# Kernel optimization log

Measured on AMD Instinct MI355X. Metric: run time of the kernel, lower is better.

Reference implementation:

```python
import jax, jax.numpy as jnp
import numpy as np

B, N, C = 16, 65536, 21          # batch, anchors, classes (class 0 = background)
TH_CONF = 0.05                   # confidence threshold
TH_IOU = 0.5                     # NMS IoU threshold
TOP_K = 200                      # candidates kept per (batch, class) before NMS
V0, V1 = 0.1, 0.2                # SSD box-coder variances


def setup_inputs() -> dict:
    key = jax.random.key(0)
    k1, k2, k3, k4 = jax.random.split(key, 4)
    conf = jax.random.normal(k1, (B, N, C), dtype=jnp.float32)
    loc = jax.random.normal(k2, (B, N, 4), dtype=jnp.float32)
    # anchors in center form (cx, cy, w, h), normalized coords
    cxcy = jax.random.uniform(k3, (N, 2), dtype=jnp.float32)
    wh = 0.02 + 0.2 * jax.random.uniform(k4, (N, 2), dtype=jnp.float32)
    anchors = jnp.concatenate([cxcy, wh], axis=-1)
    return {"conf": conf, "loc": loc, "anchors": anchors}


def _decode(anchors, loc):
    # SSD decode: anchors [N,4] center form, loc [B,N,4] offsets -> [B,N,4] xyxy
    a_xy, a_wh = anchors[:, :2], anchors[:, 2:]
    xy = a_xy + loc[..., :2] * V0 * a_wh
    wh = a_wh * jnp.exp(loc[..., 2:] * V1)
    return jnp.concatenate([xy - 0.5 * wh, xy + 0.5 * wh], axis=-1)


def _iou(boxes):
    # boxes [K,4] xyxy -> pairwise IoU [K,K]
    area = jnp.maximum(boxes[:, 2] - boxes[:, 0], 0.0) * jnp.maximum(boxes[:, 3] - boxes[:, 1], 0.0)
    lt = jnp.maximum(boxes[:, None, :2], boxes[None, :, :2])
    rb = jnp.minimum(boxes[:, None, 2:], boxes[None, :, 2:])
    wh = jnp.maximum(rb - lt, 0.0)
    inter = wh[..., 0] * wh[..., 1]
    union = area[:, None] + area[None, :] - inter
    return inter / jnp.maximum(union, 1e-9)


def _nms_keep(iou, valid):
    # greedy NMS over score-sorted candidates; valid = (score >= TH_CONF)
    K = iou.shape[0]
    idx = jnp.arange(K)

    def body(keep, xs):
        row, v, i = xs
        suppressed = jnp.any((row > TH_IOU) & keep & (idx < i))
        k = v & (~suppressed)
        return keep.at[i].set(k), 0

    keep, _ = jax.lax.scan(body, jnp.zeros((K,), dtype=bool), (iou, valid, idx))
    return keep


def reference(conf, loc, anchors):
    score = jax.nn.softmax(conf, axis=2)            # [B,N,C]
    boxes = _decode(anchors, loc)                   # [B,N,4]
    # skip background class 0 (cls_base = 1 for softmax classifier)
    cls_scores = jnp.swapaxes(score[..., 1:], 1, 2)  # [B,C-1,N]
    top_s, top_i = jax.lax.top_k(cls_scores, TOP_K)  # [B,C-1,K], sorted desc
    top_boxes = jax.vmap(lambda bx, ix: bx[ix])(boxes, top_i)  # [B,C-1,K,4]
    valid = top_s >= TH_CONF
    keep = jax.vmap(jax.vmap(lambda b, v: _nms_keep(_iou(b), v)))(top_boxes, valid)  # [B,C-1,K]
    out_boxes = jnp.where(keep[..., None], top_boxes, 0.0)
    out_scores = jnp.where(keep, top_s, 0.0)
    return jnp.concatenate([out_boxes, out_scores[..., None]], axis=-1)  # [B,C-1,K,5]
```

## Files before the change

### kernel.cpp

```cpp
#include <hip/hip_runtime.h>
#include <stdint.h>

#define NB     16
#define NANCH  65536
#define NC     21
#define NCLS   20
#define NCOL   (NB * NCLS)
#define TOPK   200
#define NBINS  1024
#define CAP    256
#define CAPCOL 4096
#define CNTSTRIDE 16
#define NPAIRS 19900

constexpr float TH      = 0.05f;
constexpr float TPRE    = 0.15f;
constexpr float SCALE15 = (float)NBINS / 0.85f;
constexpr float SCALE05 = (float)NBINS / 0.95f;

__device__ __forceinline__ int bin15(float s) {
  int b = (int)((s - 0.15f) * SCALE15);
  return b < 0 ? 0 : (b > NBINS - 1 ? NBINS - 1 : b);
}
__device__ __forceinline__ int bin05(float s) {
  int b = (int)((s - 0.05f) * SCALE05);
  return b < 0 ? 0 : (b > NBINS - 1 ? NBINS - 1 : b);
}

__device__ __forceinline__ unsigned long long shflx64(unsigned long long v, int m) {
  unsigned int lo = (unsigned int)v, hi = (unsigned int)(v >> 32);
  lo = __shfl_xor(lo, m);
  hi = __shfl_xor(hi, m);
  return ((unsigned long long)hi << 32) | lo;
}
__device__ __forceinline__ unsigned long long shfl64(unsigned long long v, int src) {
  unsigned int lo = (unsigned int)v, hi = (unsigned int)(v >> 32);
  lo = (unsigned int)__shfl((int)lo, src);
  hi = (unsigned int)__shfl((int)hi, src);
  return ((unsigned long long)hi << 32) | lo;
}

__device__ __forceinline__ void softmax_tail(const float* x, float* e, float& S) {
  float m = x[0];
#pragma unroll
  for (int c = 1; c < NC; ++c) m = fmaxf(m, x[c]);
#pragma unroll
  for (int c = 0; c < NC; ++c) e[c] = expf(x[c] - m);
  float r0 = e[0] + e[8],  r1 = e[1] + e[9],  r2 = e[2] + e[10], r3 = e[3] + e[11];
  float r4 = e[4] + e[12], r5 = e[5] + e[13], r6 = e[6] + e[14], r7 = e[7] + e[15];
  S = ((r0 + r1) + (r2 + r3)) + ((r4 + r5) + (r6 + r7));
  S += e[16]; S += e[17]; S += e[18]; S += e[19]; S += e[20];
}

__global__ __launch_bounds__(256) void softmax_collect_kernel(
    const float* __restrict__ conf,
    unsigned int* __restrict__ cnt, unsigned long long* __restrict__ cand) {
  const int tid = threadIdx.x;
  __shared__ float ld[256 * NC];
  const float4* src = (const float4*)conf + (long long)blockIdx.x * 1344;
  float4* dst4 = (float4*)ld;
#pragma unroll
  for (int i = 0; i < 5; ++i) dst4[tid + i * 256] = src[tid + i * 256];
  if (tid < 64) dst4[tid + 1280] = src[tid + 1280];
  __syncthreads();

  const int a = blockIdx.x * 256 + tid;
  const int b = a >> 16;
  const int n = a & (NANCH - 1);
  float x[NC];
#pragma unroll
  for (int c = 0; c < NC; ++c) x[c] = ld[tid * NC + c];
  float e[NC], S;
  softmax_tail(x, e, S);
  const float t = TPRE * S;
  unsigned int takemask = 0;
#pragma unroll
  for (int c = 0; c < NCLS; ++c)
    if (e[c + 1] >= t) takemask |= (1u << c);

  __shared__ unsigned int wcnt[4][NCLS];
  __shared__ unsigned int wbase[4][NCLS];
  const int wave = tid >> 6, lane = tid & 63;
#pragma unroll
  for (int c = 0; c < NCLS; ++c) {
    unsigned long long m = __ballot((takemask >> c) & 1);
    if (lane == 0) wcnt[wave][c] = (unsigned int)__popcll(m);
  }
  __syncthreads();
  if (tid < NCLS) {
    const int c = tid;
    unsigned int t0 = wcnt[0][c], t1 = wcnt[1][c], t2 = wcnt[2][c], t3 = wcnt[3][c];
    unsigned int tot = t0 + t1 + t2 + t3;
    unsigned int base = tot ? atomicAdd(&cnt[(b * NCLS + c) * CNTSTRIDE], tot) : 0u;
    wbase[0][c] = base;
    wbase[1][c] = base + t0;
    wbase[2][c] = base + t0 + t1;
    wbase[3][c] = base + t0 + t1 + t2;
  }
  __syncthreads();
#pragma unroll
  for (int c = 0; c < NCLS; ++c) {
    bool take = (takemask >> c) & 1;
    unsigned long long m = __ballot(take);
    if (take) {
      float s = e[c + 1] / S;
      unsigned int off = wbase[wave][c] +
                         (unsigned int)__popcll(m & ((1ULL << lane) - 1));
      if (off < CAPCOL) {
        unsigned int key = __float_as_uint(s) | 0x80000000u;
        cand[(long long)(b * NCLS + c) * CAPCOL + off] =
            ((unsigned long long)(key ^ 0xFFFFFFFFu) << 32) |
            (unsigned long long)(unsigned int)n;
      }
    }
  }
}

__device__ __forceinline__ int find_sel(unsigned int* hist, unsigned int* part,
                                        int* s_sel, int tid) {
  unsigned int p = hist[tid*4] + hist[tid*4+1] + hist[tid*4+2] + hist[tid*4+3];
  part[tid] = p;
  if (tid == 0) *s_sel = -1;
  __syncthreads();
  if (tid < 64) {
    unsigned int p4 = part[tid*4] + part[tid*4+1] + part[tid*4+2] + part[tid*4+3];
    unsigned int sfx = p4;
#pragma unroll
    for (int off = 1; off < 64; off <<= 1) {
      unsigned int o = __shfl_down(sfx, off);
      if (tid + off < 64) sfx += o;
    }
    unsigned int above = sfx - p4;
    if (above < TOPK && sfx >= TOPK) {
      unsigned int cum = above; int sel = tid * 16; bool found = false;
      for (int q = 3; q >= 0 && !found; --q) {
        unsigned int pc = part[tid*4 + q];
        if (cum + pc >= TOPK) {
          for (int i = 3; i >= 0; --i) {
            unsigned int c = hist[(tid*4+q)*4 + i];
            if (cum + c >= TOPK) { sel = (tid*4+q)*4 + i; found = true; break; }
            cum += c;
          }
        } else cum += pc;
      }
      *s_sel = sel;
    }
  }
  __syncthreads();
  return *s_sel;
}

__global__ __launch_bounds__(256) void topk_nms_kernel(
    const unsigned long long* __restrict__ candg,
    const unsigned int* __restrict__ cnt,
    const float* __restrict__ conf, const float* __restrict__ loc,
    const float* __restrict__ anchors, float* __restrict__ out) {
  const int bc = blockIdx.x;
  const int b  = bc / NCLS;
  const int cls = bc % NCLS;
  const int tid = threadIdx.x;

  __shared__ unsigned long long cg_lds[CAPCOL];
  __shared__ unsigned int hist[NBINS];
  __shared__ unsigned int part[256];
  __shared__ int s_sel, s_n;
  __shared__ unsigned long long cand[CAP];
  __shared__ float bx[TOPK][5];
  __shared__ float barea[TOPK];
  __shared__ unsigned long long adj[256][4];
  __shared__ unsigned long long keptw[4];

  int nc = (int)cnt[bc * CNTSTRIDE];
  const bool fast = (nc >= TOPK && nc <= CAPCOL);
  for (int i = tid; i < NBINS; i += 256) hist[i] = 0;
  if (tid == 0) s_n = 0;
#pragma unroll
  for (int w = 0; w < 4; ++w) adj[tid][w] = 0;
  __syncthreads();

  const unsigned long long* cg = candg + (long long)bc * CAPCOL;
  if (fast) {
    for (int i = tid; i < nc; i += 256) {
      unsigned long long k64 = cg[i];
      cg_lds[i] = k64;
      unsigned int key = (unsigned int)(k64 >> 32) ^ 0xFFFFFFFFu;
      float s = __uint_as_float(key ^ 0x80000000u);
      atomicAdd(&hist[bin15(s)], 1u);
    }
    __syncthreads();
    int sel = find_sel(hist, part, &s_sel, tid);
    for (int i = tid; i < nc; i += 256) {
      unsigned long long k64 = cg_lds[i];
      unsigned int key = (unsigned int)(k64 >> 32) ^ 0xFFFFFFFFu;
      float s = __uint_as_float(key ^ 0x80000000u);
      if (bin15(s) >= sel) {
        int pos = atomicAdd(&s_n, 1);
        if (pos < CAP) cand[pos] = k64;
      }
    }
  } else {
    for (int n = tid; n < NANCH; n += 256) {
      const float* row = conf + ((long long)b * NANCH + n) * NC;
      float x[NC], e[NC], S;
#pragma unroll
      for (int c = 0; c < NC; ++c) x[c] = row[c];
      softmax_tail(x, e, S);
      float s = e[cls + 1] / S;
      if (s >= TH) atomicAdd(&hist[bin05(s)], 1u);
    }
    __syncthreads();
    int sel = find_sel(hist, part, &s_sel, tid);
    for (int n = tid; n < NANCH; n += 256) {
      const float* row = conf + ((long long)b * NANCH + n) * NC;
      float x[NC], e[NC], S;
#pragma unroll
      for (int c = 0; c < NC; ++c) x[c] = row[c];
      softmax_tail(x, e, S);
      float s = e[cls + 1] / S;
      if (s >= TH && (sel < 0 || bin05(s) >= sel)) {
        int pos = atomicAdd(&s_n, 1);
        if (pos < CAP) {
          unsigned int key = __float_as_uint(s) | 0x80000000u;
          cand[pos] = ((unsigned long long)(key ^ 0xFFFFFFFFu) << 32) |
                      (unsigned long long)(unsigned int)n;
        }
      }
    }
  }
  __syncthreads();
  int ncand = s_n; if (ncand > CAP) ncand = CAP;

  unsigned long long v = (tid < ncand) ? cand[tid] : ~0ULL;
  for (int k = 2; k <= CAP; k <<= 1) {
    const bool up = ((tid & k) == 0);
    for (int j = k >> 1; j >= 64; j >>= 1) {
      cand[tid] = v;
      __syncthreads();
      unsigned long long o = cand[tid ^ j];
      bool keepMin = (((tid & j) == 0) == up);
      v = ((v < o) == keepMin) ? v : o;
      __syncthreads();
    }
    for (int j = (k >> 1) < 32 ? (k >> 1) : 32; j >= 1; j >>= 1) {
      unsigned long long o = shflx64(v, j);
      bool keepMin = (((tid & j) == 0) == up);
      v = ((v < o) == keepMin) ? v : o;
    }
  }
  const int nsel = (ncand < TOPK) ? ncand : TOPK;

  if (tid < TOPK) {
    if (tid < nsel) {
      unsigned int key = (unsigned int)(v >> 32) ^ 0xFFFFFFFFu;
      float s = __uint_as_float(key ^ 0x80000000u);
      int idx = (int)(unsigned int)(v & 0xFFFFFFFFu);
      float4 anc = ((const float4*)anchors)[idx];
      float4 l   = ((const float4*)loc)[(long long)b * NANCH + idx];
      float cx = anc.x + (l.x * 0.1f) * anc.z;
      float cy = anc.y + (l.y * 0.1f) * anc.w;
      float w  = anc.z * expf(l.z * 0.2f);
      float h  = anc.w * expf(l.w * 0.2f);
      float x1 = cx - 0.5f * w, y1 = cy - 0.5f * h;
      float x2 = cx + 0.5f * w, y2 = cy + 0.5f * h;
      bx[tid][0] = x1; bx[tid][1] = y1; bx[tid][2] = x2; bx[tid][3] = y2;
      bx[tid][4] = s;
      barea[tid] = fmaxf(x2 - x1, 0.0f) * fmaxf(y2 - y1, 0.0f);
    } else {
      bx[tid][0] = bx[tid][1] = bx[tid][2] = bx[tid][3] = bx[tid][4] = 0.0f;
      barea[tid] = 0.0f;
    }
  }
  __syncthreads();

  for (int p = tid; p < NPAIRS; p += 256) {
    float xr = (399.0f - sqrtf((float)(159201 - 8 * p))) * 0.5f;
    int i = (int)xr;
    if (i > 198) i = 198;
    while (i * (399 - i) / 2 > p) --i;
    while ((i + 1) * (398 - i) / 2 <= p) ++i;
    int j = i + 1 + (p - i * (399 - i) / 2);
    float ltx = fmaxf(bx[i][0], bx[j][0]);
    float lty = fmaxf(bx[i][1], bx[j][1]);
    float rbx = fminf(bx[i][2], bx[j][2]);
    float rby = fminf(bx[i][3], bx[j][3]);
    float iw = fmaxf(rbx - ltx, 0.0f);
    float ih = fmaxf(rby - lty, 0.0f);
    float inter = iw * ih;
    float uni = barea[i] + barea[j] - inter;
    float um = fmaxf(uni, 1e-9f);
    float half = 0.5f * um;
    bool hit;
    if (inter > half * 1.000001f)      hit = true;
    else if (inter < half * 0.999999f) hit = false;
    else                               hit = (inter / um > 0.5f);
    if (hit) atomicOr(&adj[i][j >> 6], 1ULL << (j & 63));
  }
  __syncthreads();

  if (tid < 64) {
    const int l = tid;
    unsigned long long sup1 = 0, sup2 = 0, sup3 = 0;
    unsigned long long sw;
#pragma unroll
    for (int w = 0; w < 4; ++w) {
      const int i = w * 64 + l;
      unsigned long long r0 = adj[i][0], r1 = adj[i][1],
                         r2 = adj[i][2], r3 = adj[i][3];
      sw = (w == 0) ? 0ULL : (w == 1) ? sup1 : (w == 2) ? sup2 : sup3;
      unsigned long long myintra = (w == 0) ? r0 : (w == 1) ? r1
                                 : (w == 2) ? r2 : r3;
      unsigned long long keptmask = 0;
      for (int ii = 0; ii < 64; ++ii) {
        if (((w * 64 + ii) < nsel) && !((sw >> ii) & 1ULL)) {
          keptmask |= (1ULL << ii);
          sw |= shfl64(myintra, ii);
        }
      }
      if (l == 0) keptw[w] = keptmask;
      bool mykept = (keptmask >> l) & 1ULL;
      if (w < 1) {
        unsigned long long c1 = mykept ? r1 : 0ULL;
#pragma unroll
        for (int m = 1; m < 64; m <<= 1) c1 |= shflx64(c1, m);
        sup1 |= c1;
      }
      if (w < 2) {
        unsigned long long c2 = mykept ? r2 : 0ULL;
#pragma unroll
        for (int m = 1; m < 64; m <<= 1) c2 |= shflx64(c2, m);
        sup2 |= c2;
      }
      if (w < 3) {
        unsigned long long c3 = mykept ? r3 : 0ULL;
#pragma unroll
        for (int m = 1; m < 64; m <<= 1) c3 |= shflx64(c3, m);
        sup3 |= c3;
      }
    }
  }
  __syncthreads();

  if (tid < TOPK) {
    float* o = out + ((long long)bc * TOPK + tid) * 5;
    bool k = (keptw[tid >> 6] >> (tid & 63)) & 1ULL;
    o[0] = k ? bx[tid][0] : 0.0f;
    o[1] = k ? bx[tid][1] : 0.0f;
    o[2] = k ? bx[tid][2] : 0.0f;
    o[3] = k ? bx[tid][3] : 0.0f;
    o[4] = k ? bx[tid][4] : 0.0f;
  }
}

extern "C" void kernel_launch(void* const* d_in, const int* in_sizes, int n_in,
                              void* d_out, int out_size, void* d_ws, size_t ws_size,
                              hipStream_t stream) {
  const float* conf    = (const float*)d_in[0];
  const float* loc     = (const float*)d_in[1];
  const float* anchors = (const float*)d_in[2];
  float* out = (float*)d_out;

  char* ws = (char*)d_ws;
  unsigned long long* cand = (unsigned long long*)ws;
  unsigned int*       cnt  = (unsigned int*)(ws + 10485760);

  hipMemsetAsync(ws + 10485760, 0, 320 * CNTSTRIDE * 4, stream);
  softmax_collect_kernel<<<(NB * NANCH) / 256, 256, 0, stream>>>(conf, cnt, cand);
  topk_nms_kernel<<<NCOL, 256, 0, stream>>>(cand, cnt, conf, loc, anchors, out);
}
```

Before: 103.0 us.

## Split top-k/NMS kernel into select, IoU, and greedy kernels via workspace

Splits the single per-(batch,class) top-k+NMS kernel into three launches: selection/sort/decode writing SoA boxes to workspace, an IoU kernel building the adjacency bitmask, and a 64-thread greedy kernel. The greedy pass now walks all 200 candidates serially with scalar readlane instead of shuffles and per-word OR-reductions. The aim is to shrink LDS use per kernel for better occupancy and to simplify the serial NMS. In exchange it adds two extra launches and global round trips for boxes and adjacency.

```diff
diff --git a/kernel.cpp b/kernel.cpp
--- a/kernel.cpp
+++ b/kernel.cpp
@@ -18,6 +18,13 @@
 constexpr float SCALE15 = (float)NBINS / 0.85f;
 constexpr float SCALE05 = (float)NBINS / 0.95f;
 
+#define OFF_CAND  0LL
+#define OFF_CNT   10485760LL
+#define OFF_SOA   10506240LL
+#define SOA_N     64000
+#define OFF_NSEL  12042240LL
+#define OFF_ADJ   12062720LL
+
 __device__ __forceinline__ int bin15(float s) {
   int b = (int)((s - 0.15f) * SCALE15);
   return b < 0 ? 0 : (b > NBINS - 1 ? NBINS - 1 : b);
@@ -33,10 +40,9 @@
   hi = __shfl_xor(hi, m);
   return ((unsigned long long)hi << 32) | lo;
 }
-__device__ __forceinline__ unsigned long long shfl64(unsigned long long v, int src) {
-  unsigned int lo = (unsigned int)v, hi = (unsigned int)(v >> 32);
-  lo = (unsigned int)__shfl((int)lo, src);
-  hi = (unsigned int)__shfl((int)hi, src);
+__device__ __forceinline__ unsigned long long rl64(unsigned long long v, int lane) {
+  unsigned int lo = __builtin_amdgcn_readlane((int)(unsigned int)v, lane);
+  unsigned int hi = __builtin_amdgcn_readlane((int)(unsigned int)(v >> 32), lane);
   return ((unsigned long long)hi << 32) | lo;
 }
 
@@ -150,11 +156,12 @@
   return *s_sel;
 }
 
-__global__ __launch_bounds__(256) void topk_nms_kernel(
+__global__ __launch_bounds__(256) void select_sort_decode_kernel(
     const unsigned long long* __restrict__ candg,
     const unsigned int* __restrict__ cnt,
     const float* __restrict__ conf, const float* __restrict__ loc,
-    const float* __restrict__ anchors, float* __restrict__ out) {
+    const float* __restrict__ anchors, float* __restrict__ soa,
+    int* __restrict__ nselg) {
   const int bc = blockIdx.x;
   const int b  = bc / NCLS;
   const int cls = bc % NCLS;
@@ -165,17 +172,11 @@
   __shared__ unsigned int part[256];
   __shared__ int s_sel, s_n;
   __shared__ unsigned long long cand[CAP];
-  __shared__ float bx[TOPK][5];
-  __shared__ float barea[TOPK];
-  __shared__ unsigned long long adj[256][4];
-  __shared__ unsigned long long keptw[4];
 
   int nc = (int)cnt[bc * CNTSTRIDE];
   const bool fast = (nc >= TOPK && nc <= CAPCOL);
   for (int i = tid; i < NBINS; i += 256) hist[i] = 0;
   if (tid == 0) s_n = 0;
-#pragma unroll
-  for (int w = 0; w < 4; ++w) adj[tid][w] = 0;
   __syncthreads();
 
   const unsigned long long* cg = candg + (long long)bc * CAPCOL;
@@ -250,9 +251,10 @@
   const int nsel = (ncand < TOPK) ? ncand : TOPK;
 
   if (tid < TOPK) {
+    float x1 = 0.f, y1 = 0.f, x2 = 0.f, y2 = 0.f, s = 0.f, ar = 0.f;
     if (tid < nsel) {
       unsigned int key = (unsigned int)(v >> 32) ^ 0xFFFFFFFFu;
-      float s = __uint_as_float(key ^ 0x80000000u);
+      s = __uint_as_float(key ^ 0x80000000u);
       int idx = (int)(unsigned int)(v & 0xFFFFFFFFu);
       float4 anc = ((const float4*)anchors)[idx];
       float4 l   = ((const float4*)loc)[(long long)b * NANCH + idx];
@@ -260,16 +262,37 @@
       float cy = anc.y + (l.y * 0.1f) * anc.w;
       float w  = anc.z * expf(l.z * 0.2f);
       float h  = anc.w * expf(l.w * 0.2f);
-      float x1 = cx - 0.5f * w, y1 = cy - 0.5f * h;
-      float x2 = cx + 0.5f * w, y2 = cy + 0.5f * h;
-      bx[tid][0] = x1; bx[tid][1] = y1; bx[tid][2] = x2; bx[tid][3] = y2;
-      bx[tid][4] = s;
-      barea[tid] = fmaxf(x2 - x1, 0.0f) * fmaxf(y2 - y1, 0.0f);
-    } else {
-      bx[tid][0] = bx[tid][1] = bx[tid][2] = bx[tid][3] = bx[tid][4] = 0.0f;
-      barea[tid] = 0.0f;
-    }
-  }
+      x1 = cx - 0.5f * w; y1 = cy - 0.5f * h;
+      x2 = cx + 0.5f * w; y2 = cy + 0.5f * h;
+      ar = fmaxf(x2 - x1, 0.0f) * fmaxf(y2 - y1, 0.0f);
+    }
+    int o = bc * TOPK + tid;
+    soa[0 * SOA_N + o] = x1;
+    soa[1 * SOA_N + o] = y1;
+    soa[2 * SOA_N + o] = x2;
+    soa[3 * SOA_N + o] = y2;
+    soa[4 * SOA_N + o] = s;
+    soa[5 * SOA_N + o] = ar;
+  }
+  if (tid == 0) nselg[bc * CNTSTRIDE] = nsel;
+}
+
+__global__ __launch_bounds__(256) void iou_kernel(
+    const float* __restrict__ soa, unsigned long long* __restrict__ adjg) {
+  const int bc = blockIdx.x;
+  const int tid = threadIdx.x;
+  __shared__ float x1s[TOPK], y1s[TOPK], x2s[TOPK], y2s[TOPK], ars[TOPK];
+  __shared__ unsigned long long adj[TOPK][4];
+
+  if (tid < TOPK) {
+    int o = bc * TOPK + tid;
+    x1s[tid] = soa[0 * SOA_N + o];
+    y1s[tid] = soa[1 * SOA_N + o];
+    x2s[tid] = soa[2 * SOA_N + o];
+    y2s[tid] = soa[3 * SOA_N + o];
+    ars[tid] = soa[5 * SOA_N + o];
+  }
+  for (int i = tid; i < TOPK * 4; i += 256) ((unsigned long long*)adj)[i] = 0;
   __syncthreads();
 
   for (int p = tid; p < NPAIRS; p += 256) {
@@ -279,14 +302,14 @@
     while (i * (399 - i) / 2 > p) --i;
     while ((i + 1) * (398 - i) / 2 <= p) ++i;
     int j = i + 1 + (p - i * (399 - i) / 2);
-    float ltx = fmaxf(bx[i][0], bx[j][0]);
-    float lty = fmaxf(bx[i][1], bx[j][1]);
-    float rbx = fminf(bx[i][2], bx[j][2]);
-    float rby = fminf(bx[i][3], bx[j][3]);
+    float ltx = fmaxf(x1s[i], x1s[j]);
+    float lty = fmaxf(y1s[i], y1s[j]);
+    float rbx = fminf(x2s[i], x2s[j]);
+    float rby = fminf(y2s[i], y2s[j]);
     float iw = fmaxf(rbx - ltx, 0.0f);
     float ih = fmaxf(rby - lty, 0.0f);
     float inter = iw * ih;
-    float uni = barea[i] + barea[j] - inter;
+    float uni = ars[i] + ars[j] - inter;
     float um = fmaxf(uni, 1e-9f);
     float half = 0.5f * um;
     bool hit;
@@ -296,58 +319,56 @@
     if (hit) atomicOr(&adj[i][j >> 6], 1ULL << (j & 63));
   }
   __syncthreads();
-
-  if (tid < 64) {
-    const int l = tid;
-    unsigned long long sup1 = 0, sup2 = 0, sup3 = 0;
-    unsigned long long sw;
-#pragma unroll
-    for (int w = 0; w < 4; ++w) {
-      const int i = w * 64 + l;
-      unsigned long long r0 = adj[i][0], r1 = adj[i][1],
-                         r2 = adj[i][2], r3 = adj[i][3];
-      sw = (w == 0) ? 0ULL : (w == 1) ? sup1 : (w == 2) ? sup2 : sup3;
-      unsigned long long myintra = (w == 0) ? r0 : (w == 1) ? r1
-                                 : (w == 2) ? r2 : r3;
-      unsigned long long keptmask = 0;
-      for (int ii = 0; ii < 64; ++ii) {
-        if (((w * 64 + ii) < nsel) && !((sw >> ii) & 1ULL)) {
-          keptmask |= (1ULL << ii);
-          sw |= shfl64(myintra, ii);
-        }
-      }
-      if (l == 0) keptw[w] = keptmask;
-      bool mykept = (keptmask >> l) & 1ULL;
-      if (w < 1) {
-        unsigned long long c1 = mykept ? r1 : 0ULL;
-#pragma unroll
-        for (int m = 1; m < 64; m <<= 1) c1 |= shflx64(c1, m);
-        sup1 |= c1;
-      }
-      if (w < 2) {
-        unsigned long long c2 = mykept ? r2 : 0ULL;
-#pragma unroll
-        for (int m = 1; m < 64; m <<= 1) c2 |= shflx64(c2, m);
-        sup2 |= c2;
-      }
-      if (w < 3) {
-        unsigned long long c3 = mykept ? r3 : 0ULL;
-#pragma unroll
-        for (int m = 1; m < 64; m <<= 1) c3 |= shflx64(c3, m);
-        sup3 |= c3;
-      }
-    }
-  }
-  __syncthreads();
-
-  if (tid < TOPK) {
-    float* o = out + ((long long)bc * TOPK + tid) * 5;
-    bool k = (keptw[tid >> 6] >> (tid & 63)) & 1ULL;
-    o[0] = k ? bx[tid][0] : 0.0f;
-    o[1] = k ? bx[tid][1] : 0.0f;
-    o[2] = k ? bx[tid][2] : 0.0f;
-    o[3] = k ? bx[tid][3] : 0.0f;
-    o[4] = k ? bx[tid][4] : 0.0f;
+  for (int i = tid; i < TOPK * 4; i += 256)
+    adjg[(long long)bc * (TOPK * 4) + i] = ((unsigned long long*)adj)[i];
+}
+
+__global__ __launch_bounds__(64) void greedy_out_kernel(
+    const unsigned long long* __restrict__ adjg, const int* __restrict__ nselg,
+    const float* __restrict__ soa, float* __restrict__ out) {
+  const int bc = blockIdx.x;
+  const int l  = threadIdx.x;
+  const int nsel = nselg[bc * CNTSTRIDE];
+  const unsigned long long* A = adjg + (long long)bc * (TOPK * 4);
+
+  unsigned long long r0[4], r1[4], r2[4], r3[4];
+#pragma unroll
+  for (int w = 0; w < 4; ++w) {
+    r0[w] = A[(l) * 4 + w];
+    r1[w] = A[(l + 64) * 4 + w];
+    r2[w] = (l < 72) ? A[(l + 128) * 4 + w] : 0ULL;
+    r3[w] = (l < 8)  ? A[(l + 192) * 4 + w] : 0ULL;
+  }
+  unsigned long long sup0 = 0, sup1 = 0, sup2 = 0, sup3 = 0;
+  unsigned long long k0 = 0, k1 = 0, k2 = 0, k3 = 0;
+  for (int ii = 0; ii < TOPK; ++ii) {
+    const int w = ii >> 6, bit = ii & 63;
+    unsigned long long supw = (w == 0) ? sup0 : (w == 1) ? sup1
+                            : (w == 2) ? sup2 : sup3;
+    bool kept = (ii < nsel) && !((supw >> bit) & 1ULL);
+    if (kept) {
+      unsigned long long a0, a1, a2, a3;
+      if (w == 0)      { a0=rl64(r0[0],bit); a1=rl64(r0[1],bit);
+                         a2=rl64(r0[2],bit); a3=rl64(r0[3],bit); k0 |= 1ULL<<bit; }
+      else if (w == 1) { a0=rl64(r1[0],bit); a1=rl64(r1[1],bit);
+                         a2=rl64(r1[2],bit); a3=rl64(r1[3],bit); k1 |= 1ULL<<bit; }
+      else if (w == 2) { a0=rl64(r2[0],bit); a1=rl64(r2[1],bit);
+                         a2=rl64(r2[2],bit); a3=rl64(r2[3],bit); k2 |= 1ULL<<bit; }
+      else             { a0=rl64(r3[0],bit); a1=rl64(r3[1],bit);
+                         a2=rl64(r3[2],bit); a3=rl64(r3[3],bit); k3 |= 1ULL<<bit; }
+      sup0 |= a0; sup1 |= a1; sup2 |= a2; sup3 |= a3;
+    }
+  }
+  for (int r = l; r < TOPK; r += 64) {
+    unsigned long long kw = (r < 64) ? k0 : (r < 128) ? k1 : (r < 192) ? k2 : k3;
+    bool k = (kw >> (r & 63)) & 1ULL;
+    int o = bc * TOPK + r;
+    float* po = out + (long long)o * 5;
+    po[0] = k ? soa[0 * SOA_N + o] : 0.0f;
+    po[1] = k ? soa[1 * SOA_N + o] : 0.0f;
+    po[2] = k ? soa[2 * SOA_N + o] : 0.0f;
+    po[3] = k ? soa[3 * SOA_N + o] : 0.0f;
+    po[4] = k ? soa[4 * SOA_N + o] : 0.0f;
   }
 }
 
@@ -360,10 +381,16 @@
   float* out = (float*)d_out;
 
   char* ws = (char*)d_ws;
-  unsigned long long* cand = (unsigned long long*)ws;
-  unsigned int*       cnt  = (unsigned int*)(ws + 10485760);
-
-  hipMemsetAsync(ws + 10485760, 0, 320 * CNTSTRIDE * 4, stream);
+  unsigned long long* cand  = (unsigned long long*)(ws + OFF_CAND);
+  unsigned int*       cnt   = (unsigned int*)(ws + OFF_CNT);
+  float*              soa   = (float*)(ws + OFF_SOA);
+  int*                nselg = (int*)(ws + OFF_NSEL);
+  unsigned long long* adjg  = (unsigned long long*)(ws + OFF_ADJ);
+
+  hipMemsetAsync(ws + OFF_CNT, 0, 320 * CNTSTRIDE * 4, stream);
   softmax_collect_kernel<<<(NB * NANCH) / 256, 256, 0, stream>>>(conf, cnt, cand);
-  topk_nms_kernel<<<NCOL, 256, 0, stream>>>(cand, cnt, conf, loc, anchors, out);
-}
+  select_sort_decode_kernel<<<NCOL, 256, 0, stream>>>(cand, cnt, conf, loc,
+                                                      anchors, soa, nselg);
+  iou_kernel<<<NCOL, 256, 0, stream>>>(soa, adjg);
+  greedy_out_kernel<<<NCOL, 64, 0, stream>>>(adjg, nselg, soa, out);
+}
```

New measurement: 127.8 us. 24.1% more time.

## Use per-element atomics for candidate collection and readlane-based NMS sweep

Applied to the files above, without the earlier changes.

The collect kernel drops the wave-ballot, block-level aggregation and two barriers, and instead has each thread perform one global atomicAdd per passing class to claim a slot. The NMS greedy pass now keeps all adjacency rows in registers and sweeps 200 candidates serially with scalar readlanes, replacing per-64 shuffles and butterfly OR reductions. The adj array is shrunk to TOPK rows. The trade is many more global atomics on contended counters in the collect stage against less shuffle and barrier work, and it also changes the order in which candidates are written.

```diff
diff --git a/kernel.cpp b/kernel.cpp
--- a/kernel.cpp
+++ b/kernel.cpp
@@ -33,10 +33,9 @@
   hi = __shfl_xor(hi, m);
   return ((unsigned long long)hi << 32) | lo;
 }
-__device__ __forceinline__ unsigned long long shfl64(unsigned long long v, int src) {
-  unsigned int lo = (unsigned int)v, hi = (unsigned int)(v >> 32);
-  lo = (unsigned int)__shfl((int)lo, src);
-  hi = (unsigned int)__shfl((int)hi, src);
+__device__ __forceinline__ unsigned long long rl64(unsigned long long v, int lane) {
+  unsigned int lo = __builtin_amdgcn_readlane((int)(unsigned int)v, lane);
+  unsigned int hi = __builtin_amdgcn_readlane((int)(unsigned int)(v >> 32), lane);
   return ((unsigned long long)hi << 32) | lo;
 }
 
@@ -73,45 +72,20 @@
   float e[NC], S;
   softmax_tail(x, e, S);
   const float t = TPRE * S;
-  unsigned int takemask = 0;
+  unsigned int tm = 0;
 #pragma unroll
   for (int c = 0; c < NCLS; ++c)
-    if (e[c + 1] >= t) takemask |= (1u << c);
-
-  __shared__ unsigned int wcnt[4][NCLS];
-  __shared__ unsigned int wbase[4][NCLS];
-  const int wave = tid >> 6, lane = tid & 63;
-#pragma unroll
-  for (int c = 0; c < NCLS; ++c) {
-    unsigned long long m = __ballot((takemask >> c) & 1);
-    if (lane == 0) wcnt[wave][c] = (unsigned int)__popcll(m);
-  }
-  __syncthreads();
-  if (tid < NCLS) {
-    const int c = tid;
-    unsigned int t0 = wcnt[0][c], t1 = wcnt[1][c], t2 = wcnt[2][c], t3 = wcnt[3][c];
-    unsigned int tot = t0 + t1 + t2 + t3;
-    unsigned int base = tot ? atomicAdd(&cnt[(b * NCLS + c) * CNTSTRIDE], tot) : 0u;
-    wbase[0][c] = base;
-    wbase[1][c] = base + t0;
-    wbase[2][c] = base + t0 + t1;
-    wbase[3][c] = base + t0 + t1 + t2;
-  }
-  __syncthreads();
-#pragma unroll
-  for (int c = 0; c < NCLS; ++c) {
-    bool take = (takemask >> c) & 1;
-    unsigned long long m = __ballot(take);
-    if (take) {
-      float s = e[c + 1] / S;
-      unsigned int off = wbase[wave][c] +
-                         (unsigned int)__popcll(m & ((1ULL << lane) - 1));
-      if (off < CAPCOL) {
-        unsigned int key = __float_as_uint(s) | 0x80000000u;
-        cand[(long long)(b * NCLS + c) * CAPCOL + off] =
-            ((unsigned long long)(key ^ 0xFFFFFFFFu) << 32) |
-            (unsigned long long)(unsigned int)n;
-      }
+    if (e[c + 1] >= t) tm |= (1u << c);
+
+  while (tm) {
+    int c = __builtin_ctz(tm); tm &= tm - 1;
+    float s = e[c + 1] / S;
+    unsigned int pos = atomicAdd(&cnt[(b * NCLS + c) * CNTSTRIDE], 1u);
+    if (pos < CAPCOL) {
+      unsigned int key = __float_as_uint(s) | 0x80000000u;
+      cand[(long long)(b * NCLS + c) * CAPCOL + pos] =
+          ((unsigned long long)(key ^ 0xFFFFFFFFu) << 32) |
+          (unsigned long long)(unsigned int)n;
     }
   }
 }
@@ -167,15 +141,14 @@
   __shared__ unsigned long long cand[CAP];
   __shared__ float bx[TOPK][5];
   __shared__ float barea[TOPK];
-  __shared__ unsigned long long adj[256][4];
+  __shared__ unsigned long long adj[TOPK][4];
   __shared__ unsigned long long keptw[4];
 
   int nc = (int)cnt[bc * CNTSTRIDE];
   const bool fast = (nc >= TOPK && nc <= CAPCOL);
   for (int i = tid; i < NBINS; i += 256) hist[i] = 0;
   if (tid == 0) s_n = 0;
-#pragma unroll
-  for (int w = 0; w < 4; ++w) adj[tid][w] = 0;
+  for (int i = tid; i < TOPK * 4; i += 256) ((unsigned long long*)adj)[i] = 0;
   __syncthreads();
 
   const unsigned long long* cg = candg + (long long)bc * CAPCOL;
@@ -299,44 +272,35 @@
 
   if (tid < 64) {
     const int l = tid;
-    unsigned long long sup1 = 0, sup2 = 0, sup3 = 0;
-    unsigned long long sw;
+    unsigned long long r0[4], r1[4], r2[4], r3[4];
 #pragma unroll
     for (int w = 0; w < 4; ++w) {
-      const int i = w * 64 + l;
-      unsigned long long r0 = adj[i][0], r1 = adj[i][1],
-                         r2 = adj[i][2], r3 = adj[i][3];
-      sw = (w == 0) ? 0ULL : (w == 1) ? sup1 : (w == 2) ? sup2 : sup3;
-      unsigned long long myintra = (w == 0) ? r0 : (w == 1) ? r1
-                                 : (w == 2) ? r2 : r3;
-      unsigned long long keptmask = 0;
-      for (int ii = 0; ii < 64; ++ii) {
-        if (((w * 64 + ii) < nsel) && !((sw >> ii) & 1ULL)) {
-          keptmask |= (1ULL << ii);
-          sw |= shfl64(myintra, ii);
-        }
+      r0[w] = adj[l][w];
+      r1[w] = adj[l + 64][w];
+      r2[w] = (l < 72) ? adj[l + 128][w] : 0ULL;
+      r3[w] = (l < 8)  ? adj[l + 192][w] : 0ULL;
+    }
+    unsigned long long sup0 = 0, sup1 = 0, sup2 = 0, sup3 = 0;
+    unsigned long long k0 = 0, k1 = 0, k2 = 0, k3 = 0;
+    for (int ii = 0; ii < TOPK; ++ii) {
+      const int w = ii >> 6, bit = ii & 63;
+      unsigned long long supw = (w == 0) ? sup0 : (w == 1) ? sup1
+                              : (w == 2) ? sup2 : sup3;
+      bool kept = (ii < nsel) && !((supw >> bit) & 1ULL);
+      if (kept) {
+        unsigned long long a0, a1, a2, a3;
+        if (w == 0)      { a0=rl64(r0[0],bit); a1=rl64(r0[1],bit);
+                           a2=rl64(r0[2],bit); a3=rl64(r0[3],bit); k0 |= 1ULL<<bit; }
+        else if (w == 1) { a0=rl64(r1[0],bit); a1=rl64(r1[1],bit);
+                           a2=rl64(r1[2],bit); a3=rl64(r1[3],bit); k1 |= 1ULL<<bit; }
+        else if (w == 2) { a0=rl64(r2[0],bit); a1=rl64(r2[1],bit);
+                           a2=rl64(r2[2],bit); a3=rl64(r2[3],bit); k2 |= 1ULL<<bit; }
+        else             { a0=rl64(r3[0],bit); a1=rl64(r3[1],bit);
+                           a2=rl64(r3[2],bit); a3=rl64(r3[3],bit); k3 |= 1ULL<<bit; }
+        sup0 |= a0; sup1 |= a1; sup2 |= a2; sup3 |= a3;
       }
-      if (l == 0) keptw[w] = keptmask;
-      bool mykept = (keptmask >> l) & 1ULL;
-      if (w < 1) {
-        unsigned long long c1 = mykept ? r1 : 0ULL;
-#pragma unroll
-        for (int m = 1; m < 64; m <<= 1) c1 |= shflx64(c1, m);
-        sup1 |= c1;
-      }
-      if (w < 2) {
-        unsigned long long c2 = mykept ? r2 : 0ULL;
-#pragma unroll
-        for (int m = 1; m < 64; m <<= 1) c2 |= shflx64(c2, m);
-        sup2 |= c2;
-      }
-      if (w < 3) {
-        unsigned long long c3 = mykept ? r3 : 0ULL;
-#pragma unroll
-        for (int m = 1; m < 64; m <<= 1) c3 |= shflx64(c3, m);
-        sup3 |= c3;
-      }
-    }
+    }
+    if (l == 0) { keptw[0] = k0; keptw[1] = k1; keptw[2] = k2; keptw[3] = k3; }
   }
   __syncthreads();
 
```

Result: slower. 311.5 us (+202.6%).
